# Kernel optimization log

Hardware: AMD Instinct MI355X
Metric: run time of the kernel (lower is better)

The kernel has to match this reference:

```python
import jax, jax.numpy as jnp
import numpy as np

HNM_RATIO = 10
SCALE_HW = [(160, 160), (80, 80), (40, 40)]
BATCH = 32


def _make_scale(key, b, h, w):
    k1, k2, k3, k4 = jax.random.split(key, 4)
    pred_score = jax.random.normal(k1, (b, 2, h, w), dtype=jnp.float32)
    pred_bbox = jax.random.normal(k2, (b, 4, h, w), dtype=jnp.float32)
    pos = (jax.random.uniform(k3, (b, h, w)) < 0.02).astype(jnp.float32)
    neg = 1.0 - pos
    bbox_t = jax.random.normal(k4, (b, 4, h, w), dtype=jnp.float32)
    gt_label = jnp.concatenate([pos[:, None], neg[:, None], bbox_t], axis=1)
    mask4 = jnp.broadcast_to(pos[:, None], (b, 4, h, w))
    gt_mask = jnp.concatenate([pos[:, None], neg[:, None], mask4], axis=1)
    return pred_score, pred_bbox, gt_mask, gt_label


def setup_inputs() -> dict:
    key = jax.random.key(0)
    out = {}
    for i, (h, w) in enumerate(SCALE_HW):
        ps, pb, gm, gl = _make_scale(jax.random.fold_in(key, i), BATCH, h, w)
        out[f"pred_score_{i}"] = ps
        out[f"pred_bbox_{i}"] = pb
        out[f"gt_mask_{i}"] = gm
        out[f"gt_label_{i}"] = gl
    return out


def _scale_loss(pred_score, pred_bbox, gt_mask, gt_label):
    # softmax over the 2 class channels
    sm = jax.nn.softmax(pred_score, axis=1)            # [B,2,H,W]
    log_sm = jax.nn.log_softmax(pred_score, axis=1)    # stable log(softmax)

    pos_flag = gt_label[:, 0] > 0.5                    # [B,H,W]
    neg_flag = gt_label[:, 1] > 0.5
    pos_num = jnp.sum(pos_flag.astype(jnp.float32))
    neg_num = jnp.sum(neg_flag.astype(jnp.float32))

    # hard negative mining: keep the neg_num_selected easiest negatives' quantile
    neg_sel = jnp.minimum(HNM_RATIO * pos_num, neg_num).astype(jnp.int32)
    neg_prob = jnp.where(neg_flag, sm[:, 1], 0.0)      # [B,H,W]
    neg_prob_sort = jnp.sort(neg_prob.reshape(-1))     # ascending, full sort (as in source)
    prob_threshold = neg_prob_sort[neg_sel]
    neg_grad_flag = neg_prob <= prob_threshold

    loss_mask = jnp.stack([pos_flag, neg_grad_flag], axis=1)  # [B,2,H,W] bool

    # masked cross-entropy; where(mask, -gt*log_softmax, 0) == original sum
    ce = jnp.where(loss_mask, -gt_label[:, :2] * log_sm, 0.0)
    loss_score = jnp.sum(ce) / float(ce.size)

    # masked bbox MSE; keras MeanSquaredError(SUM) = sum over all of mean over last axis
    mask_bbox = gt_mask[:, 2:6]                        # [B,4,H,W]
    diff = gt_label[:, 2:6] * mask_bbox - pred_bbox * mask_bbox
    mse_sum = jnp.sum(jnp.mean(diff * diff, axis=-1))  # mean over W, sum over rest
    loss_bbox = mse_sum / jnp.sum(mask_bbox)
    return loss_score + loss_bbox


def reference(pred_score_0, pred_bbox_0, gt_mask_0, gt_label_0,
              pred_score_1, pred_bbox_1, gt_mask_1, gt_label_1,
              pred_score_2, pred_bbox_2, gt_mask_2, gt_label_2):
    scales = [
        (pred_score_0, pred_bbox_0, gt_mask_0, gt_label_0),
        (pred_score_1, pred_bbox_1, gt_mask_1, gt_label_1),
        (pred_score_2, pred_bbox_2, gt_mask_2, gt_label_2),
    ]
    losses = [_scale_loss(*s) for s in scales]
    return jnp.stack(losses)  # [num_output_scales]
```

## Files before the change

kernel.cpp:

```cpp
#include <hip/hip_runtime.h>


namespace {
constexpr int HW0 = 25600, HW1 = 6400, HW2 = 1600;
constexpr int N0 = 32 * HW0;
constexpr int N1 = 32 * HW1;
constexpr int N2 = 32 * HW2;

constexpr int LBINS = 256;
constexpr int CAP = 8192;

constexpr int B0 = N0 / 2048, B1 = N1 / 2048, B2 = N2 / 2048;
constexpr int NBLK = B0 + B1 + B2;

__device__ __forceinline__ void scale_of(int bid, int& s, int& rel, int& lo,
                                         int& hi) {
  if (bid < B0) {
    s = 0; rel = bid; lo = 0; hi = B0;
  } else if (bid < B0 + B1) {
    s = 1; rel = bid - B0; lo = B0; hi = B0 + B1;
  } else {
    s = 2; rel = bid - B0 - B1; lo = B0 + B1; hi = NBLK;
  }
}

__device__ __forceinline__ unsigned int lin_bin(float v) {
  unsigned int b = (unsigned int)(v * 256.0f);
  return b > 255u ? 255u : b;
}
}

__global__ __launch_bounds__(256) void k_zero(uint4* __restrict__ p, int n4) {
  for (int i = threadIdx.x; i < n4; i += 256) p[i] = make_uint4(0u, 0u, 0u, 0u);
}

template <int HW>
__device__ void p1_main(int rel, const float* __restrict__ sc,
                        const float* __restrict__ bb,
                        const float* __restrict__ gl,
                        unsigned int* __restrict__ histS,
                        float* __restrict__ histceS, float* __restrict__ npvS,
                        double* __restrict__ posce_o, double* __restrict__ diff2_o,
                        unsigned int* __restrict__ pcnt_o,
                        unsigned int* __restrict__ ncnt_o) {
  __shared__ unsigned int lh[4][LBINS];
  __shared__ float lhe[4][LBINS];
  const int tid = threadIdx.x, wid = tid >> 6;
#pragma unroll
  for (int w = 0; w < 4; ++w) {
    lh[w][tid] = 0u;
    lhe[w][tid] = 0.0f;
  }
  __syncthreads();

  const int q0 = (rel * 512 + tid) * 4;
  const int q1 = q0 + 1024;
  const int bA = q0 / HW, hwA = q0 - bA * HW;
  const int bB = q1 / HW, hwB = q1 - bB * HW;
  const float* scA = sc + (size_t)bA * 2 * HW + hwA;
  const float* scB = sc + (size_t)bB * 2 * HW + hwB;
  const float* glA = gl + (size_t)bA * 6 * HW + hwA;
  const float* glB = gl + (size_t)bB * 6 * HW + hwB;
  const float4 s0A = *(const float4*)scA;
  const float4 s1A = *(const float4*)(scA + HW);
  const float4 l0A = *(const float4*)glA;
  const float4 l1A = *(const float4*)(glA + HW);
  const float4 s0B = *(const float4*)scB;
  const float4 s1B = *(const float4*)(scB + HW);
  const float4 l0B = *(const float4*)glB;
  const float4 l1B = *(const float4*)(glB + HW);

  double posce = 0.0, diff2 = 0.0;
  unsigned int pcnt = 0, ncnt = 0;

  auto process = [&](const float4& s0v, const float4& s1v, const float4& l0v,
                     const float4& l1v, const float* __restrict__ glq,
                     const float* __restrict__ bbq, float* __restrict__ npq) {
    const float s0a[4] = {s0v.x, s0v.y, s0v.z, s0v.w};
    const float s1a[4] = {s1v.x, s1v.y, s1v.z, s1v.w};
    const float l0a[4] = {l0v.x, l0v.y, l0v.z, l0v.w};
    const float l1a[4] = {l1v.x, l1v.y, l1v.z, l1v.w};
    float np[4];
#pragma unroll
    for (int j = 0; j < 4; ++j) {
      const float d = s1a[j] - s0a[j];
      const float t = expf(-fabsf(d));
      const float l1p = log1pf(t);
      const bool pos = l0a[j] > 0.5f;
      const bool neg = l1a[j] > 0.5f;
      const float sm1 = ((d >= 0.0f) ? 1.0f : t) / (1.0f + t);
      const float v = neg ? sm1 : 0.0f;
      np[j] = v;
      const unsigned int bin = lin_bin(v);
      atomicAdd(&lh[wid][bin], 1u);
      if (neg) {
        ncnt++;
        atomicAdd(&lhe[wid][bin], l1p - ((d >= 0.0f) ? 0.0f : d));
      }
      if (pos) {
        pcnt++;
        posce += (double)(-l0a[j] * (((d > 0.0f) ? -d : 0.0f) - l1p));
        float acc = 0.0f;
#pragma unroll
        for (int c = 0; c < 4; ++c) {
          const float dd = glq[(2 + c) * HW + j] - bbq[c * HW + j];
          acc += dd * dd;
        }
        diff2 += (double)acc;
      }
    }
    *(float4*)npq = make_float4(np[0], np[1], np[2], np[3]);
  };
  process(s0A, s1A, l0A, l1A, glA, bb + (size_t)bA * 4 * HW + hwA, npvS + q0);
  process(s0B, s1B, l0B, l1B, glB, bb + (size_t)bB * 4 * HW + hwB, npvS + q1);

  __syncthreads();
  {
    const unsigned int c = lh[0][tid] + lh[1][tid] + lh[2][tid] + lh[3][tid];
    if (c) atomicAdd(&histS[tid], c);
    const float e = lhe[0][tid] + lhe[1][tid] + lhe[2][tid] + lhe[3][tid];
    if (e != 0.0f) atomicAdd(&histceS[tid], e);
  }

  for (int o = 32; o > 0; o >>= 1) {
    posce += __shfl_down(posce, o, 64);
    diff2 += __shfl_down(diff2, o, 64);
    pcnt += __shfl_down(pcnt, o, 64);
    ncnt += __shfl_down(ncnt, o, 64);
  }
  __shared__ double wa[4], wb[4];
  __shared__ unsigned int wc[4], wd[4];
  if ((tid & 63) == 0) {
    wa[wid] = posce; wb[wid] = diff2; wc[wid] = pcnt; wd[wid] = ncnt;
  }
  __syncthreads();
  if (tid == 0) {
    *posce_o = wa[0] + wa[1] + wa[2] + wa[3];
    *diff2_o = wb[0] + wb[1] + wb[2] + wb[3];
    *pcnt_o = wc[0] + wc[1] + wc[2] + wc[3];
    *ncnt_o = wd[0] + wd[1] + wd[2] + wd[3];
  }
}

__global__ __launch_bounds__(256) void k_pass1(
    const float* sc0, const float* bb0, const float* gl0,
    const float* sc1, const float* bb1, const float* gl1,
    const float* sc2, const float* bb2, const float* gl2,
    unsigned int* hist, float* histce, float* npv, double* posce_a,
    double* diff2_a, unsigned int* pcnt_a, unsigned int* ncnt_a) {
  int s, rel, lo, hi;
  scale_of(blockIdx.x, s, rel, lo, hi);
  const int bid = blockIdx.x;
  if (s == 0)
    p1_main<HW0>(rel, sc0, bb0, gl0, hist, histce, npv, posce_a + bid,
                 diff2_a + bid, pcnt_a + bid, ncnt_a + bid);
  else if (s == 1)
    p1_main<HW1>(rel, sc1, bb1, gl1, hist + LBINS, histce + LBINS, npv + N0,
                 posce_a + bid, diff2_a + bid, pcnt_a + bid, ncnt_a + bid);
  else
    p1_main<HW2>(rel, sc2, bb2, gl2, hist + 2 * LBINS, histce + 2 * LBINS,
                 npv + N0 + N1, posce_a + bid, diff2_a + bid, pcnt_a + bid,
                 ncnt_a + bid);
}

__global__ __launch_bounds__(256) void k_cand(
    const unsigned int* __restrict__ pcnt_a,
    const unsigned int* __restrict__ ncnt_a,
    const unsigned int* __restrict__ hist, const float* __restrict__ npv,
    unsigned int* __restrict__ cand_cnt, unsigned int* __restrict__ cand) {
  const int tid = threadIdx.x;
  int s, rel, lo, hi;
  scale_of(blockIdx.x, s, rel, lo, hi);
  const int base = (s == 0) ? 0 : (s == 1) ? N0 : N0 + N1;

  __shared__ unsigned int sua[256], sub[256];
  {
    unsigned int c = 0, d = 0;
    for (int i = lo + tid; i < hi; i += 256) {
      c += pcnt_a[i];
      d += ncnt_a[i];
    }
    sua[tid] = c; sub[tid] = d;
  }
  __syncthreads();
  for (int o = 128; o > 0; o >>= 1) {
    if (tid < o) { sua[tid] += sua[tid + o]; sub[tid] += sub[tid + o]; }
    __syncthreads();
  }
  __shared__ unsigned int sh_k;
  if (tid == 0) {
    const unsigned long long k10 = 10ull * (unsigned long long)sua[0];
    sh_k = (k10 < (unsigned long long)sub[0]) ? (unsigned int)k10 : sub[0];
  }
  __syncthreads();

  __shared__ unsigned int partC[256];
  __shared__ unsigned int sh_selb;
  const unsigned int ownC = hist[s * LBINS + tid];
  partC[tid] = ownC;
  __syncthreads();
  for (int o = 1; o < 256; o <<= 1) {
    const unsigned int aC = (tid >= o) ? partC[tid - o] : 0u;
    __syncthreads();
    partC[tid] += aC;
    __syncthreads();
  }
  {
    const unsigned int k = sh_k;
    const unsigned int inclC = partC[tid];
    const unsigned int exclC = inclC - ownC;
    if (ownC && k >= exclC && k < inclC) sh_selb = (unsigned int)tid;
  }
  __syncthreads();

  __shared__ unsigned int cbuf[512];
  __shared__ unsigned int ccnt, cbase;
  if (tid == 0) ccnt = 0u;
  __syncthreads();
  {
    const unsigned int bsel = sh_selb;
#pragma unroll
    for (int g = 0; g < 2; ++g) {
      const int q = (rel * 512 + g * 256 + tid) * 4;
      const float4 v4 = *(const float4*)(npv + base + q);
      const float va[4] = {v4.x, v4.y, v4.z, v4.w};
#pragma unroll
      for (int j = 0; j < 4; ++j) {
        if (lin_bin(va[j]) == bsel) {
          const unsigned int sl = atomicAdd(&ccnt, 1u);
          if (sl < 512u) {
            cbuf[sl] = __float_as_uint(va[j]);
          } else {
            const unsigned int g2 = atomicAdd(&cand_cnt[s], 1u);
            if (g2 < (unsigned)CAP) cand[s * CAP + g2] = __float_as_uint(va[j]);
          }
        }
      }
    }
  }
  __syncthreads();
  if (tid == 0) {
    const unsigned int n = min(ccnt, 512u);
    cbase = n ? atomicAdd(&cand_cnt[s], n) : 0u;
  }
  __syncthreads();
  {
    const unsigned int n = min(ccnt, 512u);
    for (unsigned int i = tid; i < n; i += 256) {
      const unsigned int idx = cbase + i;
      if (idx < (unsigned)CAP) cand[s * CAP + idx] = cbuf[i];
    }
  }
}

__global__ __launch_bounds__(256) void k_select(
    const double* __restrict__ posce_a, const double* __restrict__ diff2_a,
    const unsigned int* __restrict__ pcnt_a,
    const unsigned int* __restrict__ ncnt_a,
    const unsigned int* __restrict__ hist, const float* __restrict__ histce,
    const unsigned int* __restrict__ cand_cnt,
    const unsigned int* __restrict__ cand, float* __restrict__ out) {
  const int s = blockIdx.x;
  const int tid = threadIdx.x;
  const int lo = (s == 0) ? 0 : (s == 1) ? B0 : B0 + B1;
  const int hi = (s == 0) ? B0 : (s == 1) ? B0 + B1 : NBLK;

  __shared__ double sda[256], sdb[256];
  __shared__ unsigned int sua[256], sub[256];
  {
    double a = 0.0, b2 = 0.0;
    unsigned int c = 0, d = 0;
    for (int i = lo + tid; i < hi; i += 256) {
      a += posce_a[i]; b2 += diff2_a[i];
      c += pcnt_a[i];  d += ncnt_a[i];
    }
    sda[tid] = a; sdb[tid] = b2; sua[tid] = c; sub[tid] = d;
  }
  __syncthreads();
  for (int o = 128; o > 0; o >>= 1) {
    if (tid < o) {
      sda[tid] += sda[tid + o]; sdb[tid] += sdb[tid + o];
      sua[tid] += sua[tid + o]; sub[tid] += sub[tid + o];
    }
    __syncthreads();
  }
  __shared__ double sh_posce, sh_diff2;
  __shared__ unsigned int sh_pcnt, sh_k;
  if (tid == 0) {
    sh_posce = sda[0];
    sh_diff2 = sdb[0];
    sh_pcnt = sua[0];
    const unsigned long long k10 = 10ull * (unsigned long long)sua[0];
    sh_k = (k10 < (unsigned long long)sub[0]) ? (unsigned int)k10 : sub[0];
  }
  __syncthreads();

  __shared__ unsigned int partC[256];
  __shared__ double partE[256];
  __shared__ unsigned int sh_selb, sh_selr;
  __shared__ double sh_ceb;
  const unsigned int ownC = hist[s * LBINS + tid];
  const double ownE = (double)histce[s * LBINS + tid];
  partC[tid] = ownC;
  partE[tid] = ownE;
  __syncthreads();
  for (int o = 1; o < 256; o <<= 1) {
    const unsigned int aC = (tid >= o) ? partC[tid - o] : 0u;
    const double aE = (tid >= o) ? partE[tid - o] : 0.0;
    __syncthreads();
    partC[tid] += aC;
    partE[tid] += aE;
    __syncthreads();
  }
  {
    const unsigned int k = sh_k;
    const unsigned int inclC = partC[tid];
    const unsigned int exclC = inclC - ownC;
    if (ownC && k >= exclC && k < inclC) {
      sh_selb = (unsigned int)tid;
      sh_selr = k - exclC;
      sh_ceb = partE[tid] - ownE;
    }
  }
  __syncthreads();

  const unsigned int n = min(cand_cnt[s], (unsigned int)CAP);
  const unsigned int* lst = cand + s * CAP;
  __shared__ unsigned int dh[256];
  __shared__ unsigned int shp, shr, sh_w8, sh_nr;
  if (tid == 0) {
    shr = sh_selr;
    shp = (sh_selb >= 1u) ? (lst[0] & 0xFF000000u) : 0u;
  }
  __syncthreads();
  const int r0 = (sh_selb >= 1u) ? 1 : 0;
  for (int round = r0; round < 4; ++round) {
    const int shift = 24 - 8 * round;
    dh[tid] = 0u;
    __syncthreads();
    const unsigned int pref = shp;
    for (unsigned int i = tid; i < n; i += 256) {
      const unsigned int v = lst[i];
      const bool match =
          (round == 0) || ((v >> (shift + 8)) == (pref >> (shift + 8)));
      if (match) atomicAdd(&dh[(v >> shift) & 255u], 1u);
    }
    __syncthreads();
    const unsigned int own = dh[tid];
    for (int o = 1; o < 256; o <<= 1) {
      const unsigned int add = (tid >= o) ? dh[tid - o] : 0u;
      __syncthreads();
      dh[tid] += add;
      __syncthreads();
    }
    const unsigned int incl = dh[tid];
    const unsigned int excl = incl - own;
    const unsigned int k = shr;
    if (own && k >= excl && k < incl) {
      sh_w8 = (unsigned int)tid;
      sh_nr = k - excl;
    }
    __syncthreads();
    if (tid == 0) {
      shp = pref | (sh_w8 << shift);
      shr = sh_nr;
    }
    __syncthreads();
  }
  const float thr = __uint_as_float(shp);

  double acc = 0.0;
  for (unsigned int i = tid; i < n; i += 256) {
    const float v = __uint_as_float(lst[i]);
    if (v > 0.0f && v <= thr) acc += (double)(-logf(v));
  }
  sda[tid] = acc;
  __syncthreads();
  for (int o = 128; o > 0; o >>= 1) {
    if (tid < o) sda[tid] += sda[tid + o];
    __syncthreads();
  }
  if (tid == 0) {
    const double Ns = (s == 0) ? (double)N0 : (s == 1) ? (double)N1 : (double)N2;
    const double W = (s == 0) ? 160.0 : (s == 1) ? 80.0 : 40.0;
    const double ls = (sh_posce + sh_ceb + sda[0]) / (2.0 * Ns);
    const double lb = (sh_diff2 / W) / (4.0 * (double)sh_pcnt);
    out[s] = (float)(ls + lb);
  }
}

extern "C" void kernel_launch(void* const* d_in, const int* in_sizes, int n_in,
                              void* d_out, int out_size, void* d_ws,
                              size_t ws_size, hipStream_t stream) {
  const float* sc0 = (const float*)d_in[0];
  const float* bb0 = (const float*)d_in[1];
  const float* gl0 = (const float*)d_in[3];
  const float* sc1 = (const float*)d_in[4];
  const float* bb1 = (const float*)d_in[5];
  const float* gl1 = (const float*)d_in[7];
  const float* sc2 = (const float*)d_in[8];
  const float* bb2 = (const float*)d_in[9];
  const float* gl2 = (const float*)d_in[11];

  char* ws = (char*)d_ws;
  unsigned int* hist = (unsigned int*)ws;
  float* histce = (float*)(hist + 3 * LBINS);
  unsigned int* cand_cnt = (unsigned int*)(histce + 3 * LBINS);
  size_t zbytes = (size_t)3 * LBINS * 4 * 2 + 16;
  zbytes = (zbytes + 255) & ~(size_t)255;
  size_t off = zbytes;
  double* posce_a = (double*)(ws + off);  off += (size_t)NBLK * 8;
  double* diff2_a = (double*)(ws + off);  off += (size_t)NBLK * 8;
  unsigned int* pcnt_a = (unsigned int*)(ws + off);  off += (size_t)NBLK * 4;
  unsigned int* ncnt_a = (unsigned int*)(ws + off);  off += (size_t)NBLK * 4;
  off = (off + 255) & ~(size_t)255;
  unsigned int* cand = (unsigned int*)(ws + off);
  off += (size_t)3 * CAP * 4;
  off = (off + 255) & ~(size_t)255;
  float* npv = (float*)(ws + off);

  const dim3 blk(256);
  k_zero<<<dim3(1), blk, 0, stream>>>((uint4*)d_ws, (int)(zbytes >> 4));
  k_pass1<<<dim3(NBLK), blk, 0, stream>>>(sc0, bb0, gl0, sc1, bb1, gl1, sc2,
                                          bb2, gl2, hist, histce, npv, posce_a,
                                          diff2_a, pcnt_a, ncnt_a);
  k_cand<<<dim3(NBLK), blk, 0, stream>>>(pcnt_a, ncnt_a, hist, npv, cand_cnt,
                                         cand);
  k_select<<<dim3(3), blk, 0, stream>>>(posce_a, diff2_a, pcnt_a, ncnt_a, hist,
                                        histce, cand_cnt, cand, (float*)d_out);
}
```

Measured before the change: 57.13 us.

## Recompute negative probabilities in candidate pass instead of storing intermediate buffer

```diff
diff --git a/kernel.cpp b/kernel.cpp
--- a/kernel.cpp
+++ b/kernel.cpp
@@ -39,18 +39,14 @@
                         const float* __restrict__ bb,
                         const float* __restrict__ gl,
                         unsigned int* __restrict__ histS,
-                        float* __restrict__ histceS, float* __restrict__ npvS,
-                        double* __restrict__ posce_o, double* __restrict__ diff2_o,
+                        double* __restrict__ posce_o,
+                        double* __restrict__ diff2_o,
                         unsigned int* __restrict__ pcnt_o,
                         unsigned int* __restrict__ ncnt_o) {
   __shared__ unsigned int lh[4][LBINS];
-  __shared__ float lhe[4][LBINS];
   const int tid = threadIdx.x, wid = tid >> 6;
 #pragma unroll
-  for (int w = 0; w < 4; ++w) {
-    lh[w][tid] = 0u;
-    lhe[w][tid] = 0.0f;
-  }
+  for (int w = 0; w < 4; ++w) lh[w][tid] = 0u;
   __syncthreads();
 
   const int q0 = (rel * 512 + tid) * 4;
@@ -75,12 +71,11 @@
 
   auto process = [&](const float4& s0v, const float4& s1v, const float4& l0v,
                      const float4& l1v, const float* __restrict__ glq,
-                     const float* __restrict__ bbq, float* __restrict__ npq) {
+                     const float* __restrict__ bbq) {
     const float s0a[4] = {s0v.x, s0v.y, s0v.z, s0v.w};
     const float s1a[4] = {s1v.x, s1v.y, s1v.z, s1v.w};
     const float l0a[4] = {l0v.x, l0v.y, l0v.z, l0v.w};
     const float l1a[4] = {l1v.x, l1v.y, l1v.z, l1v.w};
-    float np[4];
 #pragma unroll
     for (int j = 0; j < 4; ++j) {
       const float d = s1a[j] - s0a[j];
@@ -90,13 +85,8 @@
       const bool neg = l1a[j] > 0.5f;
       const float sm1 = ((d >= 0.0f) ? 1.0f : t) / (1.0f + t);
       const float v = neg ? sm1 : 0.0f;
-      np[j] = v;
-      const unsigned int bin = lin_bin(v);
-      atomicAdd(&lh[wid][bin], 1u);
-      if (neg) {
-        ncnt++;
-        atomicAdd(&lhe[wid][bin], l1p - ((d >= 0.0f) ? 0.0f : d));
-      }
+      atomicAdd(&lh[wid][lin_bin(v)], 1u);
+      if (neg) ncnt++;
       if (pos) {
         pcnt++;
         posce += (double)(-l0a[j] * (((d > 0.0f) ? -d : 0.0f) - l1p));
@@ -109,17 +99,14 @@
         diff2 += (double)acc;
       }
     }
-    *(float4*)npq = make_float4(np[0], np[1], np[2], np[3]);
   };
-  process(s0A, s1A, l0A, l1A, glA, bb + (size_t)bA * 4 * HW + hwA, npvS + q0);
-  process(s0B, s1B, l0B, l1B, glB, bb + (size_t)bB * 4 * HW + hwB, npvS + q1);
+  process(s0A, s1A, l0A, l1A, glA, bb + (size_t)bA * 4 * HW + hwA);
+  process(s0B, s1B, l0B, l1B, glB, bb + (size_t)bB * 4 * HW + hwB);
 
   __syncthreads();
   {
     const unsigned int c = lh[0][tid] + lh[1][tid] + lh[2][tid] + lh[3][tid];
     if (c) atomicAdd(&histS[tid], c);
-    const float e = lhe[0][tid] + lhe[1][tid] + lhe[2][tid] + lhe[3][tid];
-    if (e != 0.0f) atomicAdd(&histceS[tid], e);
   }
 
   for (int o = 32; o > 0; o >>= 1) {
@@ -146,32 +133,46 @@
     const float* sc0, const float* bb0, const float* gl0,
     const float* sc1, const float* bb1, const float* gl1,
     const float* sc2, const float* bb2, const float* gl2,
-    unsigned int* hist, float* histce, float* npv, double* posce_a,
-    double* diff2_a, unsigned int* pcnt_a, unsigned int* ncnt_a) {
+    unsigned int* hist, double* posce_a, double* diff2_a,
+    unsigned int* pcnt_a, unsigned int* ncnt_a) {
   int s, rel, lo, hi;
   scale_of(blockIdx.x, s, rel, lo, hi);
   const int bid = blockIdx.x;
   if (s == 0)
-    p1_main<HW0>(rel, sc0, bb0, gl0, hist, histce, npv, posce_a + bid,
+    p1_main<HW0>(rel, sc0, bb0, gl0, hist, posce_a + bid, diff2_a + bid,
+                 pcnt_a + bid, ncnt_a + bid);
+  else if (s == 1)
+    p1_main<HW1>(rel, sc1, bb1, gl1, hist + LBINS, posce_a + bid,
                  diff2_a + bid, pcnt_a + bid, ncnt_a + bid);
-  else if (s == 1)
-    p1_main<HW1>(rel, sc1, bb1, gl1, hist + LBINS, histce + LBINS, npv + N0,
-                 posce_a + bid, diff2_a + bid, pcnt_a + bid, ncnt_a + bid);
   else
-    p1_main<HW2>(rel, sc2, bb2, gl2, hist + 2 * LBINS, histce + 2 * LBINS,
-                 npv + N0 + N1, posce_a + bid, diff2_a + bid, pcnt_a + bid,
-                 ncnt_a + bid);
-}
-
-__global__ __launch_bounds__(256) void k_cand(
-    const unsigned int* __restrict__ pcnt_a,
-    const unsigned int* __restrict__ ncnt_a,
-    const unsigned int* __restrict__ hist, const float* __restrict__ npv,
-    unsigned int* __restrict__ cand_cnt, unsigned int* __restrict__ cand) {
+    p1_main<HW2>(rel, sc2, bb2, gl2, hist + 2 * LBINS, posce_a + bid,
+                 diff2_a + bid, pcnt_a + bid, ncnt_a + bid);
+}
+
+template <int HW>
+__device__ void p2_main(int rel, int s, int lo, int hi,
+                        const float* __restrict__ sc,
+                        const float* __restrict__ gl,
+                        const unsigned int* __restrict__ pcnt_a,
+                        const unsigned int* __restrict__ ncnt_a,
+                        const unsigned int* __restrict__ hist,
+                        double* __restrict__ ceb_o,
+                        unsigned int* __restrict__ cand_cnt,
+                        unsigned int* __restrict__ cand) {
   const int tid = threadIdx.x;
-  int s, rel, lo, hi;
-  scale_of(blockIdx.x, s, rel, lo, hi);
-  const int base = (s == 0) ? 0 : (s == 1) ? N0 : N0 + N1;
+
+  const int q0 = (rel * 512 + tid) * 4;
+  const int q1 = q0 + 1024;
+  const int bA = q0 / HW, hwA = q0 - bA * HW;
+  const int bB = q1 / HW, hwB = q1 - bB * HW;
+  const float* scA = sc + (size_t)bA * 2 * HW + hwA;
+  const float* scB = sc + (size_t)bB * 2 * HW + hwB;
+  const float4 s0A = *(const float4*)scA;
+  const float4 s1A = *(const float4*)(scA + HW);
+  const float4 l1A = *(const float4*)(gl + (size_t)bA * 6 * HW + HW + hwA);
+  const float4 s0B = *(const float4*)scB;
+  const float4 s1B = *(const float4*)(scB + HW);
+  const float4 l1B = *(const float4*)(gl + (size_t)bB * 6 * HW + HW + hwB);
 
   __shared__ unsigned int sua[256], sub[256];
   {
@@ -217,27 +218,36 @@
   __shared__ unsigned int ccnt, cbase;
   if (tid == 0) ccnt = 0u;
   __syncthreads();
-  {
-    const unsigned int bsel = sh_selb;
+  const unsigned int bsel = sh_selb;
+  double ceb = 0.0;
+
+  auto scan8 = [&](const float4& s0v, const float4& s1v, const float4& l1v) {
+    const float s0a[4] = {s0v.x, s0v.y, s0v.z, s0v.w};
+    const float s1a[4] = {s1v.x, s1v.y, s1v.z, s1v.w};
+    const float l1a[4] = {l1v.x, l1v.y, l1v.z, l1v.w};
 #pragma unroll
-    for (int g = 0; g < 2; ++g) {
-      const int q = (rel * 512 + g * 256 + tid) * 4;
-      const float4 v4 = *(const float4*)(npv + base + q);
-      const float va[4] = {v4.x, v4.y, v4.z, v4.w};
-#pragma unroll
-      for (int j = 0; j < 4; ++j) {
-        if (lin_bin(va[j]) == bsel) {
-          const unsigned int sl = atomicAdd(&ccnt, 1u);
-          if (sl < 512u) {
-            cbuf[sl] = __float_as_uint(va[j]);
-          } else {
-            const unsigned int g2 = atomicAdd(&cand_cnt[s], 1u);
-            if (g2 < (unsigned)CAP) cand[s * CAP + g2] = __float_as_uint(va[j]);
-          }
+    for (int j = 0; j < 4; ++j) {
+      const float d = s1a[j] - s0a[j];
+      const bool neg = l1a[j] > 0.5f;
+      if (!neg) continue;
+      const float t = expf(-fabsf(d));
+      const float v = ((d >= 0.0f) ? 1.0f : t) / (1.0f + t);
+      const unsigned int bin = lin_bin(v);
+      if (bin < bsel) {
+        ceb += (double)(log1pf(t) - ((d >= 0.0f) ? 0.0f : d));
+      } else if (bin == bsel) {
+        const unsigned int sl = atomicAdd(&ccnt, 1u);
+        if (sl < 512u) {
+          cbuf[sl] = __float_as_uint(v);
+        } else {
+          const unsigned int g2 = atomicAdd(&cand_cnt[s], 1u);
+          if (g2 < (unsigned)CAP) cand[s * CAP + g2] = __float_as_uint(v);
         }
       }
     }
-  }
+  };
+  scan8(s0A, s1A, l1A);
+  scan8(s0B, s1B, l1B);
   __syncthreads();
   if (tid == 0) {
     const unsigned int n = min(ccnt, 512u);
@@ -251,13 +261,40 @@
       if (idx < (unsigned)CAP) cand[s * CAP + idx] = cbuf[i];
     }
   }
+
+  for (int o = 32; o > 0; o >>= 1) ceb += __shfl_down(ceb, o, 64);
+  __shared__ double wv[4];
+  if ((tid & 63) == 0) wv[tid >> 6] = ceb;
+  __syncthreads();
+  if (tid == 0) *ceb_o = wv[0] + wv[1] + wv[2] + wv[3];
+}
+
+__global__ __launch_bounds__(256) void k_cand(
+    const float* sc0, const float* gl0, const float* sc1, const float* gl1,
+    const float* sc2, const float* gl2,
+    const unsigned int* __restrict__ pcnt_a,
+    const unsigned int* __restrict__ ncnt_a,
+    const unsigned int* __restrict__ hist, double* __restrict__ ceb_a,
+    unsigned int* __restrict__ cand_cnt, unsigned int* __restrict__ cand) {
+  int s, rel, lo, hi;
+  scale_of(blockIdx.x, s, rel, lo, hi);
+  const int bid = blockIdx.x;
+  if (s == 0)
+    p2_main<HW0>(rel, 0, lo, hi, sc0, gl0, pcnt_a, ncnt_a, hist, ceb_a + bid,
+                 cand_cnt, cand);
+  else if (s == 1)
+    p2_main<HW1>(rel, 1, lo, hi, sc1, gl1, pcnt_a, ncnt_a, hist, ceb_a + bid,
+                 cand_cnt, cand);
+  else
+    p2_main<HW2>(rel, 2, lo, hi, sc2, gl2, pcnt_a, ncnt_a, hist, ceb_a + bid,
+                 cand_cnt, cand);
 }
 
 __global__ __launch_bounds__(256) void k_select(
     const double* __restrict__ posce_a, const double* __restrict__ diff2_a,
-    const unsigned int* __restrict__ pcnt_a,
+    const double* __restrict__ ceb_a, const unsigned int* __restrict__ pcnt_a,
     const unsigned int* __restrict__ ncnt_a,
-    const unsigned int* __restrict__ hist, const float* __restrict__ histce,
+    const unsigned int* __restrict__ hist,
     const unsigned int* __restrict__ cand_cnt,
     const unsigned int* __restrict__ cand, float* __restrict__ out) {
   const int s = blockIdx.x;
@@ -265,30 +302,32 @@
   const int lo = (s == 0) ? 0 : (s == 1) ? B0 : B0 + B1;
   const int hi = (s == 0) ? B0 : (s == 1) ? B0 + B1 : NBLK;
 
-  __shared__ double sda[256], sdb[256];
+  __shared__ double sda[256], sdb[256], sdc[256];
   __shared__ unsigned int sua[256], sub[256];
   {
-    double a = 0.0, b2 = 0.0;
+    double a = 0.0, b2 = 0.0, e = 0.0;
     unsigned int c = 0, d = 0;
     for (int i = lo + tid; i < hi; i += 256) {
-      a += posce_a[i]; b2 += diff2_a[i];
+      a += posce_a[i]; b2 += diff2_a[i]; e += ceb_a[i];
       c += pcnt_a[i];  d += ncnt_a[i];
     }
-    sda[tid] = a; sdb[tid] = b2; sua[tid] = c; sub[tid] = d;
+    sda[tid] = a; sdb[tid] = b2; sdc[tid] = e; sua[tid] = c; sub[tid] = d;
   }
   __syncthreads();
   for (int o = 128; o > 0; o >>= 1) {
     if (tid < o) {
       sda[tid] += sda[tid + o]; sdb[tid] += sdb[tid + o];
+      sdc[tid] += sdc[tid + o];
       sua[tid] += sua[tid + o]; sub[tid] += sub[tid + o];
     }
     __syncthreads();
   }
-  __shared__ double sh_posce, sh_diff2;
+  __shared__ double sh_posce, sh_diff2, sh_ceb;
   __shared__ unsigned int sh_pcnt, sh_k;
   if (tid == 0) {
     sh_posce = sda[0];
     sh_diff2 = sdb[0];
+    sh_ceb = sdc[0];
     sh_pcnt = sua[0];
     const unsigned long long k10 = 10ull * (unsigned long long)sua[0];
     sh_k = (k10 < (unsigned long long)sub[0]) ? (unsigned int)k10 : sub[0];
@@ -296,20 +335,14 @@
   __syncthreads();
 
   __shared__ unsigned int partC[256];
-  __shared__ double partE[256];
   __shared__ unsigned int sh_selb, sh_selr;
-  __shared__ double sh_ceb;
   const unsigned int ownC = hist[s * LBINS + tid];
-  const double ownE = (double)histce[s * LBINS + tid];
   partC[tid] = ownC;
-  partE[tid] = ownE;
   __syncthreads();
   for (int o = 1; o < 256; o <<= 1) {
     const unsigned int aC = (tid >= o) ? partC[tid - o] : 0u;
-    const double aE = (tid >= o) ? partE[tid - o] : 0.0;
     __syncthreads();
     partC[tid] += aC;
-    partE[tid] += aE;
     __syncthreads();
   }
   {
@@ -319,7 +352,6 @@
     if (ownC && k >= exclC && k < inclC) {
       sh_selb = (unsigned int)tid;
       sh_selr = k - exclC;
-      sh_ceb = partE[tid] - ownE;
     }
   }
   __syncthreads();
@@ -404,28 +436,26 @@
 
   char* ws = (char*)d_ws;
   unsigned int* hist = (unsigned int*)ws;
-  float* histce = (float*)(hist + 3 * LBINS);
-  unsigned int* cand_cnt = (unsigned int*)(histce + 3 * LBINS);
-  size_t zbytes = (size_t)3 * LBINS * 4 * 2 + 16;
+  unsigned int* cand_cnt = hist + 3 * LBINS;
+  size_t zbytes = (size_t)3 * LBINS * 4 + 16;
   zbytes = (zbytes + 255) & ~(size_t)255;
   size_t off = zbytes;
   double* posce_a = (double*)(ws + off);  off += (size_t)NBLK * 8;
   double* diff2_a = (double*)(ws + off);  off += (size_t)NBLK * 8;
+  double* ceb_a = (double*)(ws + off);    off += (size_t)NBLK * 8;
   unsigned int* pcnt_a = (unsigned int*)(ws + off);  off += (size_t)NBLK * 4;
   unsigned int* ncnt_a = (unsigned int*)(ws + off);  off += (size_t)NBLK * 4;
   off = (off + 255) & ~(size_t)255;
   unsigned int* cand = (unsigned int*)(ws + off);
-  off += (size_t)3 * CAP * 4;
-  off = (off + 255) & ~(size_t)255;
-  float* npv = (float*)(ws + off);
 
   const dim3 blk(256);
   k_zero<<<dim3(1), blk, 0, stream>>>((uint4*)d_ws, (int)(zbytes >> 4));
   k_pass1<<<dim3(NBLK), blk, 0, stream>>>(sc0, bb0, gl0, sc1, bb1, gl1, sc2,
-                                          bb2, gl2, hist, histce, npv, posce_a,
-                                          diff2_a, pcnt_a, ncnt_a);
-  k_cand<<<dim3(NBLK), blk, 0, stream>>>(pcnt_a, ncnt_a, hist, npv, cand_cnt,
-                                         cand);
-  k_select<<<dim3(3), blk, 0, stream>>>(posce_a, diff2_a, pcnt_a, ncnt_a, hist,
-                                        histce, cand_cnt, cand, (float*)d_out);
-}
+                                          bb2, gl2, hist, posce_a, diff2_a,
+                                          pcnt_a, ncnt_a);
+  k_cand<<<dim3(NBLK), blk, 0, stream>>>(sc0, gl0, sc1, gl1, sc2, gl2, pcnt_a,
+                                         ncnt_a, hist, ceb_a, cand_cnt, cand);
+  k_select<<<dim3(3), blk, 0, stream>>>(posce_a, diff2_a, ceb_a, pcnt_a,
+                                        ncnt_a, hist, cand_cnt, cand,
+                                        (float*)d_out);
+}
```

Result: faster. 54.08 us (-5.3%).
